# Kernel optimization log

Measured on AMD Instinct MI355X. Metric: run time of the kernel, lower is better.

The kernel has to match this reference:

```python
import jax, jax.numpy as jnp
import numpy as np

HIDDEN = 4096
N_HEADS = 32
KV_HEADS = 8
HEAD_DIM = 128
GROUPS = N_HEADS // KV_HEADS
ROPE_THETA = 10000.0


def _rope_cos_sin(position_ids):
    # position_ids: [S] int -> cos/sin: [S, HEAD_DIM]
    inv_freq = 1.0 / (ROPE_THETA ** (jnp.arange(0, HEAD_DIM, 2, dtype=jnp.float32) / HEAD_DIM))
    freqs = position_ids.astype(jnp.float32)[:, None] * inv_freq[None, :]  # [S, D/2]
    emb = jnp.concatenate([freqs, freqs], axis=-1)  # [S, D]
    return jnp.cos(emb), jnp.sin(emb)


def _rotate_half(x):
    x1, x2 = jnp.split(x, 2, axis=-1)
    return jnp.concatenate([-x2, x1], axis=-1)


def _attention(hidden_states, position_ids, Wq, Wk, Wv, Wo):
    B, S, _ = hidden_states.shape
    q = hidden_states @ Wq.T  # [B,S,NH*D]
    k = hidden_states @ Wk.T  # [B,S,KVH*D]
    v = hidden_states @ Wv.T

    q = q.reshape(B, S, N_HEADS, HEAD_DIM).transpose(0, 2, 1, 3)      # [B,NH,S,D]
    k = k.reshape(B, S, KV_HEADS, HEAD_DIM).transpose(0, 2, 1, 3)     # [B,KVH,S,D]
    v = v.reshape(B, S, KV_HEADS, HEAD_DIM).transpose(0, 2, 1, 3)

    cos, sin = _rope_cos_sin(position_ids)  # [S,D]
    cos = cos[None, None]  # [1,1,S,D]
    sin = sin[None, None]
    q = q * cos + _rotate_half(q) * sin
    k = k * cos + _rotate_half(k) * sin

    # GQA expand: each kv head is repeated GROUPS times consecutively,
    # matching expand(...).reshape(...) in the torch code.
    k = jnp.repeat(k, GROUPS, axis=1)  # [B,NH,S,D]
    v = jnp.repeat(v, GROUPS, axis=1)

    scale = 1.0 / np.sqrt(HEAD_DIM)
    scores = jnp.einsum('bhqd,bhkd->bhqk', q, k) * scale  # [B,NH,S,S]
    causal = jnp.tril(jnp.ones((S, S), dtype=bool))
    scores = jnp.where(causal[None, None], scores, jnp.finfo(scores.dtype).min)
    probs = jax.nn.softmax(scores, axis=-1)
    attn = jnp.einsum('bhqk,bhkd->bhqd', probs, v)  # [B,NH,S,D]
    attn = attn.transpose(0, 2, 1, 3).reshape(B, S, N_HEADS * HEAD_DIM)
    return attn @ Wo.T


def setup_inputs() -> dict:
    key = jax.random.key(0)
    k1, k2, k3, k4, k5 = jax.random.split(key, 5)
    B, S = 2, 2048
    std = 0.02
    return {
        'hidden_states': jax.random.normal(k1, (B, S, HIDDEN), dtype=jnp.float32),
        'position_ids': jnp.arange(S, dtype=jnp.int32),
        'Wq': jax.random.normal(k2, (N_HEADS * HEAD_DIM, HIDDEN), dtype=jnp.float32) * std,
        'Wk': jax.random.normal(k3, (KV_HEADS * HEAD_DIM, HIDDEN), dtype=jnp.float32) * std,
        'Wv': jax.random.normal(k4, (KV_HEADS * HEAD_DIM, HIDDEN), dtype=jnp.float32) * std,
        'Wo': jax.random.normal(k5, (HIDDEN, N_HEADS * HEAD_DIM), dtype=jnp.float32) * std,
    }


def reference(hidden_states, position_ids, Wq, Wk, Wv, Wo):
    return _attention(hidden_states, position_ids, Wq, Wk, Wv, Wo)
```

## Files before the change

kernel.cpp:

```cpp
#include <hip/hip_runtime.h>
#include <hip/hip_bf16.h>
#include <stdint.h>


typedef uint16_t u16;
typedef __attribute__((ext_vector_type(4))) float f32x4;
typedef __attribute__((ext_vector_type(8))) short s16x8;
typedef __attribute__((ext_vector_type(4))) short s16x4;

__device__ __forceinline__ float bf2f(u16 u) {
  union { uint32_t i; float f; } v; v.i = ((uint32_t)u) << 16; return v.f;
}
__device__ __forceinline__ u16 f2bf(float f) {
  union { uint32_t i; float f; } v; v.f = f;
  uint32_t r = v.i + 0x7FFFu + ((v.i >> 16) & 1u);
  return (u16)(r >> 16);
}
__device__ __forceinline__ void gld_lds16(const void* g, void* l) {
  __builtin_amdgcn_global_load_lds((const __attribute__((address_space(1))) void*)g,
                                   (__attribute__((address_space(3))) void*)l, 16, 0, 0);
}

__global__ __launch_bounds__(256) void cvt_f32_bf16(const float* __restrict__ s,
                                                    u16* __restrict__ d, int n4) {
  int i = blockIdx.x * 256 + threadIdx.x;
  if (i < n4) {
    f32x4 v = ((const f32x4*)s)[i];
    s16x4 o;
    o.x = (short)f2bf(v.x); o.y = (short)f2bf(v.y);
    o.z = (short)f2bf(v.z); o.w = (short)f2bf(v.w);
    ((s16x4*)d)[i] = o;
  }
}

#define BM 128
#define BN 128
#define BK 64

template <typename OUT>
__global__ __launch_bounds__(256) void gemm_bt(
    const u16* __restrict__ A,
    const u16* __restrict__ B0, const u16* __restrict__ B1, const u16* __restrict__ B2,
    int nb1, int nb2,
    OUT* __restrict__ C, int K, int ldc)
{
  __shared__ u16 As[BM * BK];
  __shared__ u16 Bs[BN * BK];

  const int m0 = blockIdx.y * BM;
  const int n0 = blockIdx.x * BN;
  const u16* Bp;
  if (n0 < nb1)      Bp = B0 + (size_t)n0 * K;
  else if (n0 < nb2) Bp = B1 + (size_t)(n0 - nb1) * K;
  else               Bp = B2 + (size_t)(n0 - nb2) * K;
  const u16* Ap = A + (size_t)m0 * K;

  const int tid  = threadIdx.x;
  const int wave = tid >> 6, lane = tid & 63;
  const int wm = wave & 1, wn = wave >> 1;
  const int lr = lane & 15, lg = lane >> 4;

  const int srow = wave * 8 + (lane >> 3);
  const int scol = (lane & 7) * 8;

  f32x4 acc[4][4] = {};

  for (int k0 = 0; k0 < K; k0 += BK) {
#pragma unroll
    for (int i = 0; i < 4; i++) {
      gld_lds16(Ap + (size_t)(i * 32 + srow) * K + k0 + scol,
                (char*)As + i * 4096 + wave * 1024);
      gld_lds16(Bp + (size_t)(i * 32 + srow) * K + k0 + scol,
                (char*)Bs + i * 4096 + wave * 1024);
    }
    __syncthreads();
#pragma unroll
    for (int ks = 0; ks < 2; ks++) {
      s16x8 af[4], bf[4];
#pragma unroll
      for (int t = 0; t < 4; t++)
        af[t] = *(const s16x8*)&As[(wm * 64 + t * 16 + lr) * BK + ks * 32 + lg * 8];
#pragma unroll
      for (int t = 0; t < 4; t++)
        bf[t] = *(const s16x8*)&Bs[(wn * 64 + t * 16 + lr) * BK + ks * 32 + lg * 8];
#pragma unroll
      for (int mi = 0; mi < 4; mi++)
#pragma unroll
        for (int ni = 0; ni < 4; ni++)
          acc[mi][ni] = __builtin_amdgcn_mfma_f32_16x16x32_bf16(af[mi], bf[ni], acc[mi][ni], 0, 0, 0);
    }
    __syncthreads();
  }

  const int crow0 = m0 + wm * 64;
  const int ccol0 = n0 + wn * 64;
#pragma unroll
  for (int mi = 0; mi < 4; mi++)
#pragma unroll
    for (int ni = 0; ni < 4; ni++) {
      int col = ccol0 + ni * 16 + lr;
      int row = crow0 + mi * 16 + lg * 4;
#pragma unroll
      for (int r = 0; r < 4; r++) {
        float v = acc[mi][ni][r];
        if constexpr (sizeof(OUT) == 2)
          C[(size_t)(row + r) * ldc + col] = (OUT)f2bf(v);
        else
          C[(size_t)(row + r) * ldc + col] = (OUT)v;
      }
    }
}

__global__ __launch_bounds__(256) void rope_kernel(u16* __restrict__ qkv,
                                                   const int* __restrict__ pos_ids)
{
  int gid  = blockIdx.x * 256 + threadIdx.x;
  int pair = gid & 63;
  int u    = gid >> 6;
  int hh   = u % 40;
  int row  = u / 40;
  int s    = row & 2047;

  float p    = (float)pos_ids[s];
  float freq = exp2f(-(float)pair * 0.20762050593046014f);
  float ang  = p * freq;
  float cs   = cosf(ang), sn = sinf(ang);

  size_t base = (size_t)row * 6144 + hh * 128;
  float x1 = bf2f(qkv[base + pair]);
  float x2 = bf2f(qkv[base + pair + 64]);
  qkv[base + pair]      = f2bf(x1 * cs - x2 * sn);
  qkv[base + pair + 64] = f2bf(x2 * cs + x1 * sn);
}

#define NEGI (-30000.0f)

__global__ __launch_bounds__(256) void flash_attn(const u16* __restrict__ qkv,
                                                  u16* __restrict__ attn)
{
  __shared__ u16 Ks[64 * 136];
  __shared__ u16 Vt[128 * 64];
  __shared__ u16 Ps[4 * 32 * 72];

  const int h  = blockIdx.x;
  const int b  = blockIdx.y;
  const int qt = 15 - blockIdx.z;
  const int kvh = h >> 2;

  const int tid = threadIdx.x;
  const int wave = tid >> 6, lane = tid & 63;
  const int lr = lane & 15, lg = lane >> 4;

  const size_t rs = 6144;
  const u16* Qb = qkv + (size_t)(b * 2048) * rs + h * 128;
  const u16* Kb = qkv + (size_t)(b * 2048) * rs + 4096 + kvh * 128;
  const u16* Vb = qkv + (size_t)(b * 2048) * rs + 5120 + kvh * 128;

  s16x8 qf[2][4];
#pragma unroll
  for (int t = 0; t < 2; t++) {
    int qrow = qt * 128 + wave * 32 + t * 16 + lr;
#pragma unroll
    for (int ks = 0; ks < 4; ks++)
      qf[t][ks] = *(const s16x8*)(Qb + (size_t)qrow * rs + ks * 32 + lg * 8);
  }

  f32x4 oacc[2][8] = {};
  float mstate[2][4], lstate[2][4];
#pragma unroll
  for (int t = 0; t < 2; t++)
#pragma unroll
    for (int r = 0; r < 4; r++) { mstate[t][r] = NEGI; lstate[t][r] = 0.f; }

  const float sm_scale = 0.12751569953356377f;
  const int jmax = 2 * qt + 1;
  const int d0_s = (tid & 15) * 8;
  const int kv_s = tid >> 4;

  s16x8 kreg[4], vreg[4];
#pragma unroll
  for (int i = 0; i < 4; i++) {
    int kv = i * 16 + kv_s;
    kreg[i] = *(const s16x8*)(Kb + (size_t)kv * rs + d0_s);
    vreg[i] = *(const s16x8*)(Vb + (size_t)kv * rs + d0_s);
  }

  for (int j = 0; j <= jmax; j++) {
    __syncthreads();
#pragma unroll
    for (int i = 0; i < 4; i++) {
      int kv = i * 16 + kv_s;
      *(s16x8*)&Ks[kv * 136 + d0_s] = kreg[i];
#pragma unroll
      for (int jj = 0; jj < 8; jj++) {
        int d = d0_s + jj;
        int pk = kv ^ (((d >> 3) & 7) << 3);
        Vt[d * 64 + pk] = (u16)vreg[i][jj];
      }
    }
    __syncthreads();

    if (j < jmax) {
#pragma unroll
      for (int i = 0; i < 4; i++) {
        int kv = (j + 1) * 64 + i * 16 + kv_s;
        kreg[i] = *(const s16x8*)(Kb + (size_t)kv * rs + d0_s);
        vreg[i] = *(const s16x8*)(Vb + (size_t)kv * rs + d0_s);
      }
    }

    f32x4 sacc[2][4] = {};
#pragma unroll
    for (int ks = 0; ks < 4; ks++) {
      s16x8 kf[4];
#pragma unroll
      for (int nt = 0; nt < 4; nt++)
        kf[nt] = *(const s16x8*)&Ks[(nt * 16 + lr) * 136 + ks * 32 + lg * 8];
#pragma unroll
      for (int t = 0; t < 2; t++)
#pragma unroll
        for (int nt = 0; nt < 4; nt++)
          sacc[t][nt] = __builtin_amdgcn_mfma_f32_16x16x32_bf16(qf[t][ks], kf[nt], sacc[t][nt], 0, 0, 0);
    }

    const bool diag = (j >= 2 * qt);
#pragma unroll
    for (int t = 0; t < 2; t++) {
#pragma unroll
      for (int r = 0; r < 4; r++) {
        int qrow = qt * 128 + wave * 32 + t * 16 + lg * 4 + r;
        float mx = NEGI;
#pragma unroll
        for (int nt = 0; nt < 4; nt++) {
          float v = sacc[t][nt][r] * sm_scale;
          if (diag && (j * 64 + nt * 16 + lr) > qrow) v = NEGI;
          sacc[t][nt][r] = v;
          mx = fmaxf(mx, v);
        }
        mx = fmaxf(mx, __shfl_xor(mx, 1));
        mx = fmaxf(mx, __shfl_xor(mx, 2));
        mx = fmaxf(mx, __shfl_xor(mx, 4));
        mx = fmaxf(mx, __shfl_xor(mx, 8));
        mx = fmaxf(mx, mstate[t][r]);
        float alpha = exp2f(mstate[t][r] - mx);
        mstate[t][r] = mx;
        float rsum = 0.f;
#pragma unroll
        for (int nt = 0; nt < 4; nt++) {
          float p = exp2f(sacc[t][nt][r] - mx);
          sacc[t][nt][r] = p;
          rsum += p;
        }
        rsum += __shfl_xor(rsum, 1);
        rsum += __shfl_xor(rsum, 2);
        rsum += __shfl_xor(rsum, 4);
        rsum += __shfl_xor(rsum, 8);
        lstate[t][r] = lstate[t][r] * alpha + rsum;
#pragma unroll
        for (int n8 = 0; n8 < 8; n8++) oacc[t][n8][r] *= alpha;
#pragma unroll
        for (int nt = 0; nt < 4; nt++)
          Ps[wave * 2304 + (t * 16 + lg * 4 + r) * 72 + nt * 16 + lr] = f2bf(sacc[t][nt][r]);
      }
    }

#pragma unroll
    for (int ks2 = 0; ks2 < 2; ks2++) {
      s16x8 pf[2];
#pragma unroll
      for (int t = 0; t < 2; t++)
        pf[t] = *(const s16x8*)&Ps[wave * 2304 + (t * 16 + lr) * 72 + ks2 * 32 + lg * 8];
#pragma unroll
      for (int nt = 0; nt < 8; nt++) {
        int d = nt * 16 + lr;
        int pk = (ks2 * 32 + lg * 8) ^ (((d >> 3) & 7) << 3);
        s16x8 vf = *(const s16x8*)&Vt[d * 64 + pk];
#pragma unroll
        for (int t = 0; t < 2; t++)
          oacc[t][nt] = __builtin_amdgcn_mfma_f32_16x16x32_bf16(pf[t], vf, oacc[t][nt], 0, 0, 0);
      }
    }
  }

#pragma unroll
  for (int t = 0; t < 2; t++) {
    float inv[4];
#pragma unroll
    for (int r = 0; r < 4; r++) inv[r] = 1.0f / lstate[t][r];
    int qrow = qt * 128 + wave * 32 + t * 16 + lg * 4;
#pragma unroll
    for (int nt = 0; nt < 8; nt++) {
      int col = h * 128 + nt * 16 + lr;
#pragma unroll
      for (int r = 0; r < 4; r++)
        attn[(size_t)(b * 2048 + qrow + r) * 4096 + col] = f2bf(oacc[t][nt][r] * inv[r]);
    }
  }
}

extern "C" void kernel_launch(void* const* d_in, const int* in_sizes, int n_in,
                              void* d_out, int out_size, void* d_ws, size_t ws_size,
                              hipStream_t stream) {
  const float* X  = (const float*)d_in[0];
  const int* pos  = (const int*)d_in[1];
  const float* Wq = (const float*)d_in[2];
  const float* Wk = (const float*)d_in[3];
  const float* Wv = (const float*)d_in[4];
  const float* Wo = (const float*)d_in[5];
  float* out = (float*)d_out;

  u16* QKV = (u16*)d_ws;
  u16* Xb  = QKV + (size_t)4096 * 6144;
  u16* Wqb = Xb  + (size_t)4096 * 4096;
  u16* Wkb = Wqb + (size_t)4096 * 4096;
  u16* Wvb = Wkb + (size_t)1024 * 4096;
  u16* ATT = Xb;
  u16* Wob = Wqb;

  cvt_f32_bf16<<<16384, 256, 0, stream>>>(X,  Xb,  4194304);
  cvt_f32_bf16<<<16384, 256, 0, stream>>>(Wq, Wqb, 4194304);
  cvt_f32_bf16<<< 4096, 256, 0, stream>>>(Wk, Wkb, 1048576);
  cvt_f32_bf16<<< 4096, 256, 0, stream>>>(Wv, Wvb, 1048576);
  gemm_bt<u16><<<dim3(48, 32), 256, 0, stream>>>(Xb, Wqb, Wkb, Wvb, 4096, 5120, QKV, 4096, 6144);
  cvt_f32_bf16<<<16384, 256, 0, stream>>>(Wo, Wob, 4194304);
  rope_kernel<<<40960, 256, 0, stream>>>(QKV, pos);
  flash_attn<<<dim3(32, 2, 16), 256, 0, stream>>>(QKV, ATT);
  gemm_bt<float><<<dim3(32, 32), 256, 0, stream>>>(ATT, Wob, Wob, Wob, 1 << 30, 1 << 30, out, 4096, 4096);
}
```

Before: 1.037 ms.

## Transpose MFMA operands in flash attention so softmax rows live per lane

The flash attention kernel swaps MFMA operand order (K·Q^T and V^T·P^T), so each lane holds the scores for one query row across 16 key positions. Row max and sum then need only two cross-lane shuffles instead of four per row, P and output stores become packed 4-element writes, and the Vt LDS stride is padded from 64 to 72 to reduce bank conflicts. The cost is more LDS for Vt and a different register layout that may change register pressure.

New measurement: 914.4 us. 1.13x faster.

```diff
diff --git a/kernel.cpp b/kernel.cpp
--- a/kernel.cpp
+++ b/kernel.cpp
@@ -134,13 +134,15 @@
 }
 
 #define NEGI (-30000.0f)
+#define VTS 72
+#define PSS 72
 
 __global__ __launch_bounds__(256) void flash_attn(const u16* __restrict__ qkv,
                                                   u16* __restrict__ attn)
 {
   __shared__ u16 Ks[64 * 136];
-  __shared__ u16 Vt[128 * 64];
-  __shared__ u16 Ps[4 * 32 * 72];
+  __shared__ u16 Vt[128 * VTS];
+  __shared__ u16 Ps[4 * 32 * PSS];
 
   const int h  = blockIdx.x;
   const int b  = blockIdx.y;
@@ -158,19 +160,17 @@
 
   s16x8 qf[2][4];
 #pragma unroll
-  for (int t = 0; t < 2; t++) {
-    int qrow = qt * 128 + wave * 32 + t * 16 + lr;
+  for (int nt = 0; nt < 2; nt++) {
+    int qrow = qt * 128 + wave * 32 + nt * 16 + lr;
 #pragma unroll
     for (int ks = 0; ks < 4; ks++)
-      qf[t][ks] = *(const s16x8*)(Qb + (size_t)qrow * rs + ks * 32 + lg * 8);
-  }
-
-  f32x4 oacc[2][8] = {};
-  float mstate[2][4], lstate[2][4];
-#pragma unroll
-  for (int t = 0; t < 2; t++)
-#pragma unroll
-    for (int r = 0; r < 4; r++) { mstate[t][r] = NEGI; lstate[t][r] = 0.f; }
+      qf[nt][ks] = *(const s16x8*)(Qb + (size_t)qrow * rs + ks * 32 + lg * 8);
+  }
+
+  f32x4 oacc[8][2] = {};
+  float mstate[2], lstate[2];
+#pragma unroll
+  for (int nt = 0; nt < 2; nt++) { mstate[nt] = NEGI; lstate[nt] = 0.f; }
 
   const float sm_scale = 0.12751569953356377f;
   const int jmax = 2 * qt + 1;
@@ -195,7 +195,7 @@
       for (int jj = 0; jj < 8; jj++) {
         int d = d0_s + jj;
         int pk = kv ^ (((d >> 3) & 7) << 3);
-        Vt[d * 64 + pk] = (u16)vreg[i][jj];
+        Vt[d * VTS + pk] = (u16)vreg[i][jj];
       }
     }
     __syncthreads();
@@ -209,91 +209,105 @@
       }
     }
 
-    f32x4 sacc[2][4] = {};
+    f32x4 sacc[4][2] = {};
 #pragma unroll
     for (int ks = 0; ks < 4; ks++) {
       s16x8 kf[4];
 #pragma unroll
-      for (int nt = 0; nt < 4; nt++)
-        kf[nt] = *(const s16x8*)&Ks[(nt * 16 + lr) * 136 + ks * 32 + lg * 8];
-#pragma unroll
-      for (int t = 0; t < 2; t++)
-#pragma unroll
-        for (int nt = 0; nt < 4; nt++)
-          sacc[t][nt] = __builtin_amdgcn_mfma_f32_16x16x32_bf16(qf[t][ks], kf[nt], sacc[t][nt], 0, 0, 0);
+      for (int mt = 0; mt < 4; mt++)
+        kf[mt] = *(const s16x8*)&Ks[(mt * 16 + lr) * 136 + ks * 32 + lg * 8];
+#pragma unroll
+      for (int mt = 0; mt < 4; mt++)
+#pragma unroll
+        for (int nt = 0; nt < 2; nt++)
+          sacc[mt][nt] = __builtin_amdgcn_mfma_f32_16x16x32_bf16(kf[mt], qf[nt][ks], sacc[mt][nt], 0, 0, 0);
     }
 
     const bool diag = (j >= 2 * qt);
 #pragma unroll
-    for (int t = 0; t < 2; t++) {
-#pragma unroll
-      for (int r = 0; r < 4; r++) {
-        int qrow = qt * 128 + wave * 32 + t * 16 + lg * 4 + r;
-        float mx = NEGI;
-#pragma unroll
-        for (int nt = 0; nt < 4; nt++) {
-          float v = sacc[t][nt][r] * sm_scale;
-          if (diag && (j * 64 + nt * 16 + lr) > qrow) v = NEGI;
-          sacc[t][nt][r] = v;
-          mx = fmaxf(mx, v);
+    for (int nt = 0; nt < 2; nt++) {
+      const int qg = qt * 128 + wave * 32 + nt * 16 + lr;
+      float p[16];
+#pragma unroll
+      for (int mt = 0; mt < 4; mt++)
+#pragma unroll
+        for (int r = 0; r < 4; r++) {
+          float v = sacc[mt][nt][r] * sm_scale;
+          int kvg = j * 64 + mt * 16 + lg * 4 + r;
+          if (diag && kvg > qg) v = NEGI;
+          p[mt * 4 + r] = v;
         }
-        mx = fmaxf(mx, __shfl_xor(mx, 1));
-        mx = fmaxf(mx, __shfl_xor(mx, 2));
-        mx = fmaxf(mx, __shfl_xor(mx, 4));
-        mx = fmaxf(mx, __shfl_xor(mx, 8));
-        mx = fmaxf(mx, mstate[t][r]);
-        float alpha = exp2f(mstate[t][r] - mx);
-        mstate[t][r] = mx;
-        float rsum = 0.f;
-#pragma unroll
-        for (int nt = 0; nt < 4; nt++) {
-          float p = exp2f(sacc[t][nt][r] - mx);
-          sacc[t][nt][r] = p;
-          rsum += p;
-        }
-        rsum += __shfl_xor(rsum, 1);
-        rsum += __shfl_xor(rsum, 2);
-        rsum += __shfl_xor(rsum, 4);
-        rsum += __shfl_xor(rsum, 8);
-        lstate[t][r] = lstate[t][r] * alpha + rsum;
-#pragma unroll
-        for (int n8 = 0; n8 < 8; n8++) oacc[t][n8][r] *= alpha;
-#pragma unroll
-        for (int nt = 0; nt < 4; nt++)
-          Ps[wave * 2304 + (t * 16 + lg * 4 + r) * 72 + nt * 16 + lr] = f2bf(sacc[t][nt][r]);
-      }
-    }
-
-#pragma unroll
-    for (int ks2 = 0; ks2 < 2; ks2++) {
+      float mx;
+      {
+        float a0 = fmaxf(fmaxf(p[0], p[1]), fmaxf(p[2], p[3]));
+        float a1 = fmaxf(fmaxf(p[4], p[5]), fmaxf(p[6], p[7]));
+        float a2 = fmaxf(fmaxf(p[8], p[9]), fmaxf(p[10], p[11]));
+        float a3 = fmaxf(fmaxf(p[12], p[13]), fmaxf(p[14], p[15]));
+        mx = fmaxf(fmaxf(a0, a1), fmaxf(a2, a3));
+      }
+      mx = fmaxf(mx, __shfl_xor(mx, 16));
+      mx = fmaxf(mx, __shfl_xor(mx, 32));
+      mx = fmaxf(mx, mstate[nt]);
+      float alpha = exp2f(mstate[nt] - mx);
+      mstate[nt] = mx;
+      float e[16];
+      float rsum;
+#pragma unroll
+      for (int i = 0; i < 16; i++) e[i] = exp2f(p[i] - mx);
+      {
+        float s0 = (e[0] + e[1]) + (e[2] + e[3]);
+        float s1 = (e[4] + e[5]) + (e[6] + e[7]);
+        float s2 = (e[8] + e[9]) + (e[10] + e[11]);
+        float s3 = (e[12] + e[13]) + (e[14] + e[15]);
+        rsum = (s0 + s1) + (s2 + s3);
+      }
+      rsum += __shfl_xor(rsum, 16);
+      rsum += __shfl_xor(rsum, 32);
+      lstate[nt] = lstate[nt] * alpha + rsum;
+#pragma unroll
+      for (int dt = 0; dt < 8; dt++)
+        oacc[dt][nt] *= alpha;
+#pragma unroll
+      for (int mt = 0; mt < 4; mt++) {
+        s16x4 pk4;
+        pk4.x = (short)f2bf(e[mt * 4 + 0]);
+        pk4.y = (short)f2bf(e[mt * 4 + 1]);
+        pk4.z = (short)f2bf(e[mt * 4 + 2]);
+        pk4.w = (short)f2bf(e[mt * 4 + 3]);
+        *(s16x4*)&Ps[wave * (32 * PSS) + (nt * 16 + lr) * PSS + mt * 16 + lg * 4] = pk4;
+      }
+    }
+
+#pragma unroll
+    for (int c = 0; c < 2; c++) {
       s16x8 pf[2];
 #pragma unroll
-      for (int t = 0; t < 2; t++)
-        pf[t] = *(const s16x8*)&Ps[wave * 2304 + (t * 16 + lr) * 72 + ks2 * 32 + lg * 8];
-#pragma unroll
-      for (int nt = 0; nt < 8; nt++) {
-        int d = nt * 16 + lr;
-        int pk = (ks2 * 32 + lg * 8) ^ (((d >> 3) & 7) << 3);
-        s16x8 vf = *(const s16x8*)&Vt[d * 64 + pk];
-#pragma unroll
-        for (int t = 0; t < 2; t++)
-          oacc[t][nt] = __builtin_amdgcn_mfma_f32_16x16x32_bf16(pf[t], vf, oacc[t][nt], 0, 0, 0);
-      }
-    }
-  }
-
-#pragma unroll
-  for (int t = 0; t < 2; t++) {
-    float inv[4];
-#pragma unroll
-    for (int r = 0; r < 4; r++) inv[r] = 1.0f / lstate[t][r];
-    int qrow = qt * 128 + wave * 32 + t * 16 + lg * 4;
-#pragma unroll
-    for (int nt = 0; nt < 8; nt++) {
-      int col = h * 128 + nt * 16 + lr;
-#pragma unroll
-      for (int r = 0; r < 4; r++)
-        attn[(size_t)(b * 2048 + qrow + r) * 4096 + col] = f2bf(oacc[t][nt][r] * inv[r]);
+      for (int nt = 0; nt < 2; nt++)
+        pf[nt] = *(const s16x8*)&Ps[wave * (32 * PSS) + (nt * 16 + lr) * PSS + c * 32 + lg * 8];
+#pragma unroll
+      for (int dt = 0; dt < 8; dt++) {
+        int d = dt * 16 + lr;
+        int kv0 = (c * 32 + lg * 8) ^ (((d >> 3) & 7) << 3);
+        s16x8 vf = *(const s16x8*)&Vt[d * VTS + kv0];
+#pragma unroll
+        for (int nt = 0; nt < 2; nt++)
+          oacc[dt][nt] = __builtin_amdgcn_mfma_f32_16x16x32_bf16(vf, pf[nt], oacc[dt][nt], 0, 0, 0);
+      }
+    }
+  }
+
+#pragma unroll
+  for (int nt = 0; nt < 2; nt++) {
+    float inv = 1.0f / lstate[nt];
+    int qrow = b * 2048 + qt * 128 + wave * 32 + nt * 16 + lr;
+#pragma unroll
+    for (int dt = 0; dt < 8; dt++) {
+      s16x4 o4;
+      o4.x = (short)f2bf(oacc[dt][nt][0] * inv);
+      o4.y = (short)f2bf(oacc[dt][nt][1] * inv);
+      o4.z = (short)f2bf(oacc[dt][nt][2] * inv);
+      o4.w = (short)f2bf(oacc[dt][nt][3] * inv);
+      *(s16x4*)&attn[(size_t)qrow * 4096 + h * 128 + dt * 16 + lg * 4] = o4;
     }
   }
 }
```
